# Optimization experiments

Hardware: AMD Instinct MI355X
Metric: run time of the kernel (lower is better)

## Reference

```python
import jax, jax.numpy as jnp
import numpy as np

K_NODES = 512  # per-expert capacity (k_nodes init arg)


def setup_inputs() -> dict:
    key = jax.random.key(0)
    k1, k2, k3, k4 = jax.random.split(key, 4)
    B_T, D, E = 16384, 512, 64
    x = jax.random.normal(k1, (B_T, D, 2), jnp.float32)
    # gate: orthogonal_(gain=0.1) ~ small-scale dense matrix
    gate_weights = jax.random.normal(k2, (2 * D, E), jnp.float32) * (0.1 / np.sqrt(2 * D))
    # ComplexKaimingInitializer: |N(0,1)|/sqrt(fan_in) magnitude, uniform phase
    mag = jnp.abs(jax.random.normal(k3, (E, D, D), jnp.float32)) / np.sqrt(D)
    phase = jax.random.uniform(k4, (E, D, D), jnp.float32, minval=0.0, maxval=2.0 * np.pi)
    experts_w = jnp.stack([mag * jnp.cos(phase), mag * jnp.sin(phase)], axis=-1)  # [E,D,D,2]
    act_bias = jnp.zeros((D,), jnp.float32)
    return {"x": x, "gate_weights": gate_weights, "experts_w": experts_w, "act_bias": act_bias}


def reference(x, gate_weights, experts_w, act_bias):
    # x: [B_T, D, 2] interleaved-real tokens
    B_T, D, _ = x.shape
    E = gate_weights.shape[1]
    k = min(B_T, K_NODES)

    # --- expert-choice routing: each expert picks its top-k tokens ---
    scores = jnp.nan_to_num(x.reshape(B_T, 2 * D) @ gate_weights)  # [B_T, E]
    topk_scores, topk_idx = jax.lax.top_k(scores.T, k)             # [E, k] each

    # --- gather tokens per expert (row-major [E, k] order, as in forward()) ---
    flat_gather = topk_idx.reshape(-1)                  # [E*k]
    xb = x[flat_gather].reshape(E, k, D, 2)             # [E, k, D, 2]
    xr, xi = xb[..., 0], xb[..., 1]
    wr, wi = experts_w[..., 0], experts_w[..., 1]

    # --- grouped complex GEMM as 4 real batched matmuls ---
    yr = jnp.einsum('ekd,edf->ekf', xr, wr) - jnp.einsum('ekd,edf->ekf', xi, wi)
    yi = jnp.einsum('ekd,edf->ekf', xr, wi) + jnp.einsum('ekd,edf->ekf', xi, wr)
    y = jnp.nan_to_num(jnp.stack([yr, yi], axis=-1))    # [E, k, D, 2]

    # weight by routing scores, then scatter-add combine
    y_weighted = (y * topk_scores[..., None, None]).reshape(E * k, D, 2)
    # NOTE: original code scatters with topk_indices.T.reshape(-1) (column-major
    # w.r.t. the [E,k] gather order). Reproduced faithfully.
    flat_scatter = topk_idx.T.reshape(-1)               # [E*k]
    out = jnp.zeros((B_T, D, 2), jnp.float32).at[flat_scatter].add(y_weighted)
    counts = jnp.zeros((B_T,), jnp.float32).at[flat_scatter].add(1.0)
    agg = out / jnp.maximum(counts, 1.0)[:, None, None]

    # ComplexGELU: exact (erf) GELU on real/imag parts with shared bias
    res = jax.nn.gelu(agg + act_bias[:, None], approximate=False)  # [B_T, D, 2]
    return res
```

## Files before the change

kernel.cpp:

```cpp
#include <hip/hip_runtime.h>
#include <stdint.h>
#include <math.h>

typedef uint32_t u32;
typedef uint64_t u64;
typedef unsigned short u16;

#define B_T    16384
#define DD     512
#define NE     64
#define KCAP   512
#define TWO_D  1024

typedef __attribute__((ext_vector_type(8))) short bf16x8;
typedef __attribute__((ext_vector_type(4))) float f32x4;
typedef __attribute__((ext_vector_type(4))) u32 u32x4;

static __device__ __forceinline__ u32 mono_of(float s) {
  u32 b = __float_as_uint(s);
  return (b & 0x80000000u) ? ~b : (b | 0x80000000u);
}
static __device__ __forceinline__ float score_from_mono(u32 m) {
  u32 b = (m & 0x80000000u) ? (m ^ 0x80000000u) : ~m;
  return __uint_as_float(b);
}
static __device__ __forceinline__ u16 f2bf(float f) {
  u32 b = __float_as_uint(f);
  b += 0x7FFFu + ((b >> 16) & 1u);
  return (u16)(b >> 16);
}
static __device__ __forceinline__ u32 f2bf2(float lo, float hi) {
  return (u32)f2bf(lo) | ((u32)f2bf(hi) << 16);
}
static __device__ __forceinline__ float bf2f(u32 u) {
  return __uint_as_float(u << 16);
}
static __device__ __forceinline__ u32 cvtpk(float lo, float hi) {
  u32 r;
  asm("v_cvt_pk_bf16_f32 %0, %1, %2" : "=v"(r) : "v"(lo), "v"(hi));
  return r;
}
static __device__ __forceinline__ void gload_lds16(const u16* g, u16* l) {
  __builtin_amdgcn_global_load_lds(
      (const __attribute__((address_space(1))) u32*)(g),
      (__attribute__((address_space(3))) u32*)(l), 16, 0, 0);
}
static __device__ __forceinline__ bf16x8 negbf8(bf16x8 v) {
  u32x4 u;
  u32x4 s = *reinterpret_cast<u32x4*>(&v);
  u[0] = s[0] ^ 0x80008000u;
  u[1] = s[1] ^ 0x80008000u;
  u[2] = s[2] ^ 0x80008000u;
  u[3] = s[3] ^ 0x80008000u;
  return *reinterpret_cast<bf16x8*>(&u);
}

__global__ __launch_bounds__(256) void k1_gate(const float* __restrict__ x,
                                               const float* __restrict__ gw,
                                               float* __restrict__ scoresT,
                                               u16* __restrict__ xrb,
                                               u16* __restrict__ xib) {
  __shared__ __align__(16) float xs[128][32];
  __shared__ __align__(16) float gs[128][64];
  const int tb  = blockIdx.x * 32;
  const int tid = threadIdx.x;
  const int tx = tid & 7, ty = tid >> 3;

  float accC[2][4];
  float accT[2][4];
#pragma unroll
  for (int i = 0; i < 2; ++i)
#pragma unroll
    for (int j = 0; j < 4; ++j) { accC[i][j] = 0.f; accT[i][j] = 0.f; }

  for (int c = 0; c < 8; ++c) {
    const int k0 = c * 128;
    {
      const int t = tid & 31, ks = (tid >> 5) * 16;
      const float* src = x + (size_t)(tb + t) * TWO_D + k0 + ks;
      u32 rr[4], ii[4];
#pragma unroll
      for (int i = 0; i < 4; ++i) {
        float4 v = reinterpret_cast<const float4*>(src)[i];
        xs[ks + i * 4 + 0][t] = v.x;
        xs[ks + i * 4 + 1][t] = v.y;
        xs[ks + i * 4 + 2][t] = v.z;
        xs[ks + i * 4 + 3][t] = v.w;
        rr[i] = f2bf2(v.x, v.z);
        ii[i] = f2bf2(v.y, v.w);
      }
      const size_t xoff = (size_t)(tb + t) * 512 + c * 64 + (ks >> 1);
      uint4 wr, wi;
      wr.x = rr[0]; wr.y = rr[1]; wr.z = rr[2]; wr.w = rr[3];
      wi.x = ii[0]; wi.y = ii[1]; wi.z = ii[2]; wi.w = ii[3];
      *reinterpret_cast<uint4*>(xrb + xoff) = wr;
      *reinterpret_cast<uint4*>(xib + xoff) = wi;

      const float4* gsrc = reinterpret_cast<const float4*>(gw + (size_t)k0 * 64);
      float4* gdst = reinterpret_cast<float4*>(&gs[0][0]);
#pragma unroll
      for (int i = 0; i < 8; ++i) gdst[tid + i * 256] = gsrc[tid + i * 256];
    }
    __syncthreads();
    for (int k = 0; k < 128; ++k) {
      float4 a4 = *reinterpret_cast<float4*>(&xs[k][tx * 4]);
      float2 b2 = *reinterpret_cast<float2*>(&gs[k][ty * 2]);
      float av[4] = {a4.x, a4.y, a4.z, a4.w};
      float bv[2] = {b2.x, b2.y};
#pragma unroll
      for (int i = 0; i < 2; ++i)
#pragma unroll
        for (int j = 0; j < 4; ++j) accC[i][j] = fmaf(bv[i], av[j], accC[i][j]);
    }
    __syncthreads();
    if (c == 3 || c == 7) {
#pragma unroll
      for (int i = 0; i < 2; ++i)
#pragma unroll
        for (int j = 0; j < 4; ++j) {
          accT[i][j] = accT[i][j] + accC[i][j];
          accC[i][j] = 0.f;
        }
    }
  }
#pragma unroll
  for (int i = 0; i < 2; ++i) {
    float4 v = make_float4(accT[i][0], accT[i][1], accT[i][2], accT[i][3]);
    *reinterpret_cast<float4*>(&scoresT[(size_t)(ty * 2 + i) * B_T + tb + tx * 4]) = v;
  }
}

__global__ __launch_bounds__(1024) void k2_topk(const float* __restrict__ scoresT,
                                                int* __restrict__ topk_idx,
                                                float* __restrict__ topk_scr,
                                                int* __restrict__ counts,
                                                int* __restrict__ entries) {
  const int e = blockIdx.x, tid = threadIdx.x;
  const float* row = scoresT + (size_t)e * B_T;
  __shared__ u32 keys[B_T];
  __shared__ u32 hist[256];
  __shared__ u32 s_prefix, s_r;
  __shared__ u32 cnt_gt, cnt_eq;
  __shared__ u64 skey[512];
  __shared__ u32 tie[512];

#pragma unroll
  for (int i = 0; i < 4; ++i) {
    int v4 = i * 1024 + tid;
    float4 v = reinterpret_cast<const float4*>(row)[v4];
    keys[v4 * 4 + 0] = mono_of(v.x);
    keys[v4 * 4 + 1] = mono_of(v.y);
    keys[v4 * 4 + 2] = mono_of(v.z);
    keys[v4 * 4 + 3] = mono_of(v.w);
  }
  if (tid == 0) { s_prefix = 0; s_r = KCAP; cnt_gt = 0; cnt_eq = 0; }
  u32 prefmask = 0;
  __syncthreads();

  for (int pass = 0; pass < 4; ++pass) {
    const int shift = 24 - 8 * pass;
    if (tid < 256) hist[tid] = 0;
    __syncthreads();
    const u32 prefix = s_prefix;
    for (int t = tid; t < B_T; t += 1024) {
      u32 m = keys[t];
      if ((m & prefmask) == prefix) atomicAdd(&hist[(m >> shift) & 0xFFu], 1u);
    }
    __syncthreads();
    if (tid == 0) {
      u32 r = s_r, cum = 0;
      int sel = 0;
      for (int b = 255; b >= 0; --b) {
        if (cum + hist[b] >= r) { sel = b; s_r = r - cum; break; }
        cum += hist[b];
      }
      s_prefix = prefix | ((u32)sel << shift);
    }
    prefmask |= (0xFFu << shift);
    __syncthreads();
  }

  const u32 kmono = s_prefix;
  const u32 rneed = s_r;

  for (int t = tid; t < B_T; t += 1024) {
    u32 m = keys[t];
    if (m > kmono) {
      u32 p = atomicAdd(&cnt_gt, 1u);
      if (p < 512) skey[p] = ((u64)(~m) << 32) | (u32)t;
    } else if (m == kmono) {
      u32 p = atomicAdd(&cnt_eq, 1u);
      if (p < 512) tie[p] = (u32)t;
    }
  }
  __syncthreads();

  const u32 ngt = cnt_gt;
  const u32 ne = cnt_eq < 512u ? cnt_eq : 512u;
  if (tid < ne) {
    u32 my = tie[tid];
    u32 rank = 0;
    for (u32 j = 0; j < ne; ++j) rank += (tie[j] < my) ? 1u : 0u;
    if (rank < rneed) skey[ngt + rank] = ((u64)(~kmono) << 32) | my;
  }
  __syncthreads();

  if (tid < 512) {
    u64 my = skey[tid];
    u32 rank = 0;
    for (int j = 0; j < 512; ++j) rank += (skey[j] < my) ? 1u : 0u;
    u32 idx = (u32)my;
    u32 m = ~((u32)(my >> 32));
    topk_idx[e * KCAP + rank] = (int)idx;
    topk_scr[e * KCAP + rank] = score_from_mono(m);
    int pos = atomicAdd(&counts[idx], 1);
    entries[idx * 64 + pos] = (int)(rank * 64 + e);
  }
}

__global__ __launch_bounds__(256) void k3_wtrans(const float* __restrict__ w,
                                                 u16* __restrict__ wrT,
                                                 u16* __restrict__ wiT) {
  __shared__ float fr[64][33];
  __shared__ float fi[64][33];
  const int bid = blockIdx.x;
  const int e = bid >> 7, tile = bid & 127;
  const int d0 = (tile >> 4) * 64, f0 = (tile & 15) * 32;
  const int tid = threadIdx.x;
  {
    const int row = tid >> 2, lane4 = tid & 3;
    const float* src = w + ((size_t)(e * 512 + d0 + row)) * 1024 + f0 * 2 + lane4 * 16;
#pragma unroll
    for (int i = 0; i < 4; ++i) {
      float4 v = reinterpret_cast<const float4*>(src)[i];
      int fl = lane4 * 8 + 2 * i;
      fr[row][fl] = v.x;      fi[row][fl] = v.y;
      fr[row][fl + 1] = v.z;  fi[row][fl + 1] = v.w;
    }
  }
  __syncthreads();
  {
    const int f = tid >> 3, dg = tid & 7;
    u32 pr[4], pi[4];
#pragma unroll
    for (int j = 0; j < 4; ++j) {
      float r0 = fr[dg * 8 + 2 * j][f],     i0 = fi[dg * 8 + 2 * j][f];
      float r1 = fr[dg * 8 + 2 * j + 1][f], i1 = fi[dg * 8 + 2 * j + 1][f];
      pr[j] = f2bf2(r0, r1);
      pi[j] = f2bf2(i0, i1);
    }
    const size_t off = ((size_t)e * 512 + f0 + f) * 512 + d0 + dg * 8;
    uint4 vr, vi;
    vr.x = pr[0]; vr.y = pr[1]; vr.z = pr[2]; vr.w = pr[3];
    vi.x = pi[0]; vi.y = pi[1]; vi.z = pi[2]; vi.w = pi[3];
    *reinterpret_cast<uint4*>(wrT + off) = vr;
    *reinterpret_cast<uint4*>(wiT + off) = vi;
  }
}

__global__ __launch_bounds__(256, 2) void k4_pre(
    const u16* __restrict__ xrb, const u16* __restrict__ xib,
    const int* __restrict__ topk_idx, const float* __restrict__ topk_scr,
    const u16* __restrict__ wrT, const u16* __restrict__ wiT,
    u16* __restrict__ yrw, u16* __restrict__ yiw) {
  const int bid = blockIdx.x;
  const int xcd = bid & 7, q = bid >> 3, t = q & 15, g = q >> 4;
  const int e = g * 8 + xcd;
  const int mb = t & 3, fb = t >> 2;
  const int m0 = mb * 128, f0 = fb * 128;

  __shared__ __align__(16) u16 Ar[4096];
  __shared__ __align__(16) u16 Ai[4096];
  __shared__ __align__(16) u16 Bu[4096];
  __shared__ __align__(16) u16 Bv[4096];
  __shared__ int tok[128];
  __shared__ float scr[128];

  const int tid = threadIdx.x;
  if (tid < 128) {
    tok[tid] = topk_idx[e * KCAP + m0 + tid];
    scr[tid] = topk_scr[e * KCAP + m0 + tid];
  }
  __syncthreads();

  const int r0  = tid & 127;
  const int ka0 = (tid >> 7) * 8;
  const int ka1 = ka0 + 16;
  const size_t brow = ((size_t)e * 512 + f0 + r0) * 512;
  const size_t arow = (size_t)tok[r0] * 512;
  const int wv = tid >> 6, ln = tid & 63;
  const int d0 = wv * 512;
  const int d1 = 2048 + wv * 512;

  const int mbase = (wv >> 1) * 64, nbase = (wv & 1) * 64;
  const int frow = ln & 15, fq = ln >> 4;
  const int ra = fq * 1024 + (mbase + frow) * 8;
  const int rb = fq * 1024 + (nbase + frow) * 8;

  f32x4 accR[4][4] = {};
  f32x4 accI[4][4] = {};

  for (int step = 0; step < 16; ++step) {
    const int k0 = step * 32;
    gload_lds16(wrT + brow + k0 + ka0, Bu + d0);
    gload_lds16(wrT + brow + k0 + ka1, Bu + d1);
    gload_lds16(wiT + brow + k0 + ka0, Bv + d0);
    gload_lds16(wiT + brow + k0 + ka1, Bv + d1);
    gload_lds16(xrb + arow + k0 + ka0, Ar + d0);
    gload_lds16(xrb + arow + k0 + ka1, Ar + d1);
    gload_lds16(xib + arow + k0 + ka0, Ai + d0);
    gload_lds16(xib + arow + k0 + ka1, Ai + d1);
    __syncthreads();

    bf16x8 ar[4], ai[4], bu[4], bv[4];
#pragma unroll
    for (int m = 0; m < 4; ++m) {
      ar[m] = *reinterpret_cast<const bf16x8*>(&Ar[ra + m * 128]);
      ai[m] = *reinterpret_cast<const bf16x8*>(&Ai[ra + m * 128]);
    }
#pragma unroll
    for (int n = 0; n < 4; ++n) {
      bu[n] = *reinterpret_cast<const bf16x8*>(&Bu[rb + n * 128]);
      bv[n] = *reinterpret_cast<const bf16x8*>(&Bv[rb + n * 128]);
    }
#pragma unroll
    for (int m = 0; m < 4; ++m)
#pragma unroll
      for (int n = 0; n < 4; ++n) {
        bf16x8 bw = negbf8(bv[n]);
        accR[m][n] = __builtin_amdgcn_mfma_f32_16x16x32_bf16(ar[m], bu[n], accR[m][n], 0, 0, 0);
        accR[m][n] = __builtin_amdgcn_mfma_f32_16x16x32_bf16(ai[m], bw,    accR[m][n], 0, 0, 0);
        accI[m][n] = __builtin_amdgcn_mfma_f32_16x16x32_bf16(ar[m], bv[n], accI[m][n], 0, 0, 0);
        accI[m][n] = __builtin_amdgcn_mfma_f32_16x16x32_bf16(ai[m], bu[n], accI[m][n], 0, 0, 0);
      }
    __syncthreads();
  }

  const int rr = fq * 4;
#pragma unroll
  for (int m = 0; m < 4; ++m) {
#pragma unroll
    for (int r = 0; r < 4; ++r) {
      const int jl = mbase + m * 16 + rr + r;
      const float ww = scr[jl];
      const size_t ybase = ((size_t)e * KCAP + m0 + jl) * DD;
#pragma unroll
      for (int n = 0; n < 4; ++n) {
        const int fg = f0 + nbase + n * 16 + frow;
        yrw[ybase + fg] = f2bf(accR[m][n][r] * ww);
        yiw[ybase + fg] = f2bf(accI[m][n][r] * ww);
      }
    }
  }
}

__global__ __launch_bounds__(256, 2) void k4_fb(
    const float* __restrict__ x, const int* __restrict__ topk_idx,
    const float* __restrict__ topk_scr, const u16* __restrict__ wrT,
    const u16* __restrict__ wiT, u16* __restrict__ yrw, u16* __restrict__ yiw) {
  const int bid = blockIdx.x;
  const int xcd = bid & 7, q = bid >> 3, t = q & 15, g = q >> 4;
  const int e = g * 8 + xcd;
  const int mb = t & 3, fb = t >> 2;
  const int m0 = mb * 128, f0 = fb * 128;

  __shared__ __align__(16) u16 Ar[4096];
  __shared__ __align__(16) u16 Ai[4096];
  __shared__ __align__(16) u16 Bu[4096];
  __shared__ __align__(16) u16 Bv[4096];
  __shared__ int tok[128];
  __shared__ float scr[128];

  const int tid = threadIdx.x;
  if (tid < 128) {
    tok[tid] = topk_idx[e * KCAP + m0 + tid];
    scr[tid] = topk_scr[e * KCAP + m0 + tid];
  }
  __syncthreads();

  const int r0  = tid & 127;
  const int ka0 = (tid >> 7) * 8;
  const int ka1 = ka0 + 16;
  const size_t brow = ((size_t)e * 512 + f0 + r0) * 512;
  const int wv = tid >> 6, ln = tid & 63;
  const int d0 = wv * 512;
  const int d1 = 2048 + wv * 512;

  const int row = tid >> 1, half = tid & 1;
  const float* arow_f = x + (size_t)tok[row] * TWO_D + half * 32;

  const int mbase = (wv >> 1) * 64, nbase = (wv & 1) * 64;
  const int frow = ln & 15, fq = ln >> 4;
  const int ra = fq * 1024 + (mbase + frow) * 8;
  const int rb = fq * 1024 + (nbase + frow) * 8;

  f32x4 accR[4][4] = {};
  f32x4 accI[4][4] = {};

  for (int step = 0; step < 16; ++step) {
    const int k0 = step * 32;
    gload_lds16(wrT + brow + k0 + ka0, Bu + d0);
    gload_lds16(wrT + brow + k0 + ka1, Bu + d1);
    gload_lds16(wiT + brow + k0 + ka0, Bv + d0);
    gload_lds16(wiT + brow + k0 + ka1, Bv + d1);
    {
      const float4* ap = reinterpret_cast<const float4*>(arow_f + (size_t)k0 * 2);
      u32 xr[8], xi[8];
#pragma unroll
      for (int i = 0; i < 8; ++i) {
        float4 v = ap[i];
        xr[i] = cvtpk(v.x, v.z);
        xi[i] = cvtpk(v.y, v.w);
      }
      uint4 wa, wb;
      wa.x = xr[0]; wa.y = xr[1]; wa.z = xr[2]; wa.w = xr[3];
      wb.x = xr[4]; wb.y = xr[5]; wb.z = xr[6]; wb.w = xr[7];
      *reinterpret_cast<uint4*>(&Ar[(2 * half) * 1024 + row * 8]) = wa;
      *reinterpret_cast<uint4*>(&Ar[(2 * half + 1) * 1024 + row * 8]) = wb;
      wa.x = xi[0]; wa.y = xi[1]; wa.z = xi[2]; wa.w = xi[3];
      wb.x = xi[4]; wb.y = xi[5]; wb.z = xi[6]; wb.w = xi[7];
      *reinterpret_cast<uint4*>(&Ai[(2 * half) * 1024 + row * 8]) = wa;
      *reinterpret_cast<uint4*>(&Ai[(2 * half + 1) * 1024 + row * 8]) = wb;
    }
    __syncthreads();

    bf16x8 ar[4], ai[4], bu[4], bv[4];
#pragma unroll
    for (int m = 0; m < 4; ++m) {
      ar[m] = *reinterpret_cast<const bf16x8*>(&Ar[ra + m * 128]);
      ai[m] = *reinterpret_cast<const bf16x8*>(&Ai[ra + m * 128]);
    }
#pragma unroll
    for (int n = 0; n < 4; ++n) {
      bu[n] = *reinterpret_cast<const bf16x8*>(&Bu[rb + n * 128]);
      bv[n] = *reinterpret_cast<const bf16x8*>(&Bv[rb + n * 128]);
    }
#pragma unroll
    for (int m = 0; m < 4; ++m)
#pragma unroll
      for (int n = 0; n < 4; ++n) {
        bf16x8 bw = negbf8(bv[n]);
        accR[m][n] = __builtin_amdgcn_mfma_f32_16x16x32_bf16(ar[m], bu[n], accR[m][n], 0, 0, 0);
        accR[m][n] = __builtin_amdgcn_mfma_f32_16x16x32_bf16(ai[m], bw,    accR[m][n], 0, 0, 0);
        accI[m][n] = __builtin_amdgcn_mfma_f32_16x16x32_bf16(ar[m], bv[n], accI[m][n], 0, 0, 0);
        accI[m][n] = __builtin_amdgcn_mfma_f32_16x16x32_bf16(ai[m], bu[n], accI[m][n], 0, 0, 0);
      }
    __syncthreads();
  }

  const int rr = fq * 4;
#pragma unroll
  for (int m = 0; m < 4; ++m) {
#pragma unroll
    for (int r = 0; r < 4; ++r) {
      const int jl = mbase + m * 16 + rr + r;
      const float ww = scr[jl];
      const size_t ybase = ((size_t)e * KCAP + m0 + jl) * DD;
#pragma unroll
      for (int n = 0; n < 4; ++n) {
        const int fg = f0 + nbase + n * 16 + frow;
        yrw[ybase + fg] = f2bf(accR[m][n][r] * ww);
        yiw[ybase + fg] = f2bf(accI[m][n][r] * ww);
      }
    }
  }
}

#define GELU(z) (0.5f * (z) * (1.0f + erff((z)*0.70710678118654752440f)))
__global__ __launch_bounds__(256) void k5_gather(
    const u16* __restrict__ yrw, const u16* __restrict__ yiw,
    const int* __restrict__ counts, const int* __restrict__ entries,
    const float* __restrict__ bias, float* __restrict__ out) {
  const int t = blockIdx.x * 2 + (threadIdx.x >> 7);
  const int lane = threadIdx.x & 127;
  const int c = counts[t];
  const float inv = 1.0f / (float)(c > 0 ? c : 1);
  const int f4 = lane * 4;
  float sr[4] = {0.f, 0.f, 0.f, 0.f}, si[4] = {0.f, 0.f, 0.f, 0.f};
  for (int i = 0; i < c; ++i) {
    int srcrow = entries[t * 64 + i];
    size_t off = (size_t)srcrow * DD + f4;
    uint2 pr = *reinterpret_cast<const uint2*>(yrw + off);
    uint2 pi = *reinterpret_cast<const uint2*>(yiw + off);
    sr[0] += bf2f(pr.x & 0xFFFFu); sr[1] += bf2f(pr.x >> 16);
    sr[2] += bf2f(pr.y & 0xFFFFu); sr[3] += bf2f(pr.y >> 16);
    si[0] += bf2f(pi.x & 0xFFFFu); si[1] += bf2f(pi.x >> 16);
    si[2] += bf2f(pi.y & 0xFFFFu); si[3] += bf2f(pi.y >> 16);
  }
  const float b0 = bias[f4], b1 = bias[f4 + 1], b2 = bias[f4 + 2], b3 = bias[f4 + 3];
  float4 o1, o2;
  o1.x = GELU(sr[0] * inv + b0); o1.y = GELU(si[0] * inv + b0);
  o1.z = GELU(sr[1] * inv + b1); o1.w = GELU(si[1] * inv + b1);
  o2.x = GELU(sr[2] * inv + b2); o2.y = GELU(si[2] * inv + b2);
  o2.z = GELU(sr[3] * inv + b3); o2.w = GELU(si[3] * inv + b3);
  float* dst = out + (size_t)t * TWO_D + (size_t)f4 * 2;
  reinterpret_cast<float4*>(dst)[0] = o1;
  reinterpret_cast<float4*>(dst)[1] = o2;
}

extern "C" void kernel_launch(void* const* d_in, const int* in_sizes, int n_in,
                              void* d_out, int out_size, void* d_ws, size_t ws_size,
                              hipStream_t stream) {
  const float* x    = (const float*)d_in[0];
  const float* gw   = (const float*)d_in[1];
  const float* w    = (const float*)d_in[2];
  const float* bias = (const float*)d_in[3];
  float* out = (float*)d_out;

  char* ws = (char*)d_ws;
  u16*   yrw     = (u16*)(ws);
  float* scoresT = (float*)(ws);
  u16*   yiw     = (u16*)(ws + 33554432);
  int*   tidx    = (int*)(ws + 67108864);
  float* tscr    = (float*)(ws + 67239936);
  int*   counts  = (int*)(ws + 67371008);
  int*   entries = (int*)(ws + 67436544);
  u16*   wrT     = (u16*)(ws + 71630848);
  u16*   wiT     = (u16*)(ws + 105185280);
  u16*   xrb     = (u16*)(ws + 138739712);
  u16*   xib     = (u16*)(ws + 155516928);

  const bool preconv = ws_size >= 172294144ull;

  hipMemsetAsync(counts, 0, B_T * sizeof(int), stream);
  if (preconv) {
    k1_gate<<<B_T / 32, 256, 0, stream>>>(x, gw, scoresT, xrb, xib);
    k2_topk<<<NE, 1024, 0, stream>>>(scoresT, tidx, tscr, counts, entries);
    k3_wtrans<<<NE * 128, 256, 0, stream>>>(w, wrT, wiT);
    k4_pre<<<1024, 256, 0, stream>>>(xrb, xib, tidx, tscr, wrT, wiT, yrw, yiw);
  } else {
    k1_gate<<<B_T / 32, 256, 0, stream>>>(x, gw, scoresT, (u16*)(ws + 33554432),
                                          (u16*)(ws + 33554432 + 16777216));
    k2_topk<<<NE, 1024, 0, stream>>>(scoresT, tidx, tscr, counts, entries);
    k3_wtrans<<<NE * 128, 256, 0, stream>>>(w, wrT, wiT);
    k4_fb<<<1024, 256, 0, stream>>>(x, tidx, tscr, wrT, wiT, yrw, yiw);
  }
  k5_gather<<<B_T / 2, 256, 0, stream>>>(yrw, yiw, counts, entries, bias, out);
}
```

Measured before the change: 276.8 us.

## Stage k4_pre epilogue through LDS for coalesced 16-byte stores; raise occupancy hint

The k4_pre epilogue used to write each bf16 output element to global memory as a scattered 2-byte store. It now writes the scaled results into the reused shared-memory tile buffer and then emits coalesced uint4 stores, first for the real half and then for the imaginary half. The launch bounds also go from 2 to 4 blocks per SM. The cost is extra barriers and LDS traffic, and the higher occupancy target may force register spilling given the 32 accumulator vectors.

```diff
diff --git a/kernel.cpp b/kernel.cpp
--- a/kernel.cpp
+++ b/kernel.cpp
@@ -258,7 +258,7 @@
   }
 }
 
-__global__ __launch_bounds__(256, 2) void k4_pre(
+__global__ __launch_bounds__(256, 4) void k4_pre(
     const u16* __restrict__ xrb, const u16* __restrict__ xib,
     const int* __restrict__ topk_idx, const float* __restrict__ topk_scr,
     const u16* __restrict__ wrT, const u16* __restrict__ wiT,
@@ -269,10 +269,11 @@
   const int mb = t & 3, fb = t >> 2;
   const int m0 = mb * 128, f0 = fb * 128;
 
-  __shared__ __align__(16) u16 Ar[4096];
-  __shared__ __align__(16) u16 Ai[4096];
-  __shared__ __align__(16) u16 Bu[4096];
-  __shared__ __align__(16) u16 Bv[4096];
+  __shared__ __align__(16) u16 buf[16384];
+  u16* Ar = buf;
+  u16* Ai = buf + 4096;
+  u16* Bu = buf + 8192;
+  u16* Bv = buf + 12288;
   __shared__ int tok[128];
   __shared__ float scr[128];
 
@@ -337,20 +338,43 @@
   }
 
   const int rr = fq * 4;
-#pragma unroll
-  for (int m = 0; m < 4; ++m) {
+  const size_t yrow0 = ((size_t)e * KCAP + m0);
+#pragma unroll
+  for (int m = 0; m < 4; ++m)
 #pragma unroll
     for (int r = 0; r < 4; ++r) {
       const int jl = mbase + m * 16 + rr + r;
       const float ww = scr[jl];
-      const size_t ybase = ((size_t)e * KCAP + m0 + jl) * DD;
-#pragma unroll
-      for (int n = 0; n < 4; ++n) {
-        const int fg = f0 + nbase + n * 16 + frow;
-        yrw[ybase + fg] = f2bf(accR[m][n][r] * ww);
-        yiw[ybase + fg] = f2bf(accI[m][n][r] * ww);
-      }
-    }
+#pragma unroll
+      for (int n = 0; n < 4; ++n)
+        buf[jl * 128 + nbase + n * 16 + frow] = f2bf(accR[m][n][r] * ww);
+    }
+  __syncthreads();
+#pragma unroll
+  for (int i = 0; i < 8; ++i) {
+    const int idx = i * 256 + tid;
+    const int row = idx >> 4, col = idx & 15;
+    uint4 v = *reinterpret_cast<const uint4*>(&buf[row * 128 + col * 8]);
+    *reinterpret_cast<uint4*>(&yrw[(yrow0 + row) * DD + f0 + col * 8]) = v;
+  }
+  __syncthreads();
+#pragma unroll
+  for (int m = 0; m < 4; ++m)
+#pragma unroll
+    for (int r = 0; r < 4; ++r) {
+      const int jl = mbase + m * 16 + rr + r;
+      const float ww = scr[jl];
+#pragma unroll
+      for (int n = 0; n < 4; ++n)
+        buf[jl * 128 + nbase + n * 16 + frow] = f2bf(accI[m][n][r] * ww);
+    }
+  __syncthreads();
+#pragma unroll
+  for (int i = 0; i < 8; ++i) {
+    const int idx = i * 256 + tid;
+    const int row = idx >> 4, col = idx & 15;
+    uint4 v = *reinterpret_cast<const uint4*>(&buf[row * 128 + col * 8]);
+    *reinterpret_cast<uint4*>(&yiw[(yrow0 + row) * DD + f0 + col * 8]) = v;
   }
 }
 
```

Result: slower. 835.3 us (+201.8%).
